# Optimization experiments

Hardware: AMD Instinct MI355X
Metric: run time of the kernel (lower is better)

Reference implementation:

```python
import jax, jax.numpy as jnp
import numpy as np

N = 16384
E = 262144
HID = 128
NFILT = 128
NGAUSS = 50
NINTER = 6
CUTOFF = 10.0
NUMZ = 100
LOG2 = 0.6931471805599453


def ssp(x):
    # ShiftedSoftplus
    return jax.nn.softplus(x) - LOG2


def setup_inputs() -> dict:
    key = jax.random.key(0)
    ks = jax.random.split(key, 20)
    z = jax.random.randint(ks[0], (N,), 0, NUMZ)
    pos = jax.random.uniform(ks[1], (N, 3), dtype=jnp.float32) * 5.0  # box side 5 -> all pairs < cutoff
    edge_index = jax.random.randint(ks[2], (2, E), 0, N)
    s = lambda k, shape, fan: jax.random.normal(k, shape, dtype=jnp.float32) / np.sqrt(fan)
    params = dict(
        emb=s(ks[3], (NUMZ, HID), 1.0),
        Wf1=s(ks[4], (NINTER, NGAUSS, NFILT), NGAUSS), bf1=jnp.zeros((NINTER, NFILT), jnp.float32),
        Wf2=s(ks[5], (NINTER, NFILT, NFILT), NFILT), bf2=jnp.zeros((NINTER, NFILT), jnp.float32),
        Wl1=s(ks[6], (NINTER, HID, NFILT), HID),
        Wl2=s(ks[7], (NINTER, NFILT, HID), NFILT), bl2=jnp.zeros((NINTER, HID), jnp.float32),
        Wl=s(ks[8], (NINTER, HID, HID), HID), bl=jnp.zeros((NINTER, HID), jnp.float32),
        Wo1=s(ks[9], (HID, HID // 2), HID), bo1=jnp.zeros((HID // 2,), jnp.float32),
        Wo2=s(ks[10], (HID // 2, 1), HID // 2), bo2=jnp.zeros((1,), jnp.float32),
    )
    return dict(z=z, pos=pos, edge_index=edge_index, **params)


def reference(z, pos, edge_index, emb, Wf1, bf1, Wf2, bf2, Wl1, Wl2, bl2, Wl, bl, Wo1, bo1, Wo2, bo2):
    src, dst = edge_index[0], edge_index[1]
    # edge distances and Gaussian smearing
    d = jnp.linalg.norm(pos[src] - pos[dst], axis=-1)          # [E]
    offset = jnp.linspace(0.0, CUTOFF, NGAUSS, dtype=jnp.float32)
    coeff = -0.5 / (offset[1] - offset[0]) ** 2
    ea = jnp.exp(coeff * (d[:, None] - offset) ** 2)            # [E, NGAUSS]
    C = 0.5 * (jnp.cos(d * (np.pi / CUTOFF)) + 1.0)             # cosine cutoff [E]

    h = emb[z]                                                  # [N, HID]
    for i in range(NINTER):
        # continuous-filter weights
        Wfilt = (ssp(ea @ Wf1[i] + bf1[i]) @ Wf2[i] + bf2[i]) * C[:, None]  # [E, NFILT]
        x = h @ Wl1[i]                                          # lin1, no bias [N, NFILT]
        msg = x[src] * Wfilt                                    # gather + filter
        agg = jax.ops.segment_sum(msg, dst, num_segments=N)     # scatter-sum [N, NFILT]
        x = ssp(agg @ Wl2[i] + bl2[i]) @ Wl[i] + bl[i]          # lin2 -> ssp -> lin
        h = h + x

    h = ssp(h @ Wo1 + bo1) @ Wo2 + bo2                          # [N, 1] per-atom energy
    out = jnp.sum(h, axis=0, keepdims=True)                     # 'add' readout, single graph -> [1, 1]
    return jax.nn.relu(out)
```

## Files before the change

### kernel.cpp

```cpp
#include <hip/hip_runtime.h>
#include <math.h>

#define NATOM 16384
#define NEDGE 262144
#define HID 128
#define NG 50
#define NI 6

typedef _Float16 h8_t __attribute__((ext_vector_type(8)));
typedef _Float16 h4_t __attribute__((ext_vector_type(4)));
typedef float    f4_t __attribute__((ext_vector_type(4)));

__device__ __forceinline__ float ssp_f(float v) {
    float e = __expf(-fabsf(v));
    return fmaxf(v, 0.0f) + __logf(1.0f + e) - 0.69314718055994531f;
}

__global__ void fill0(float* __restrict__ p, int n4) {
    int i = blockIdx.x * 256 + threadIdx.x;
    if (i < n4) ((float4*)p)[i] = make_float4(0.f, 0.f, 0.f, 0.f);
}

__global__ void hist_k(const int* __restrict__ ei, int* __restrict__ cnt) {
    int e = blockIdx.x * 256 + threadIdx.x;
    if (e < NEDGE) atomicAdd(&cnt[ei[NEDGE + e]], 1);
}

__global__ void scan_k(const int* __restrict__ cnt, int* __restrict__ offs) {
    __shared__ int part[256];
    int t = threadIdx.x;
    int base = t * 64;
    int s = 0;
    for (int i = 0; i < 64; ++i) s += cnt[base + i];
    part[t] = s;
    __syncthreads();
    for (int off = 1; off < 256; off <<= 1) {
        int v = (t >= off) ? part[t - off] : 0;
        __syncthreads();
        part[t] += v;
        __syncthreads();
    }
    int r = part[t] - s;
    for (int i = 0; i < 64; ++i) { offs[base + i] = r; r += cnt[base + i]; }
    if (t == 255) offs[NATOM] = r;
}

__global__ void scatter_k(const int* __restrict__ ei, const int* __restrict__ offs,
                          int* __restrict__ cnt, int* __restrict__ sSrc, int* __restrict__ sDst) {
    int e = blockIdx.x * 256 + threadIdx.x;
    if (e >= NEDGE) return;
    int d = ei[NEDGE + e];
    int r = atomicAdd(&cnt[d], 1);
    int j = offs[d] + r;
    sSrc[j] = ei[e];
    sDst[j] = d;
}

__global__ void edge_pre(const float* __restrict__ pos,
                         const int* __restrict__ sSrc, const int* __restrict__ sDst,
                         _Float16* __restrict__ eaH, _Float16* __restrict__ eaL,
                         float* __restrict__ Cb) {
    int j = blockIdx.x * 256 + threadIdx.x;
    if (j >= NEDGE) return;
    int s = sSrc[j], dd = sDst[j];
    float dx = pos[3*s]   - pos[3*dd];
    float dy = pos[3*s+1] - pos[3*dd+1];
    float dz = pos[3*s+2] - pos[3*dd+2];
    float d = sqrtf(dx*dx + dy*dy + dz*dz);
    Cb[j] = 0.5f * (cosf(d * 0.31415926535897931f) + 1.0f);
    const float delta = 10.0f / 49.0f;
    const float coeff = -0.5f / (delta * delta);
    #pragma unroll
    for (int gq = 0; gq < 8; ++gq) {
        h8_t hv, lv;
        #pragma unroll
        for (int r = 0; r < 8; ++r) {
            int g = gq * 8 + r;
            float v = 0.0f;
            if (g < NG) { float u = d - (float)g * delta; v = __expf(coeff * u * u); }
            _Float16 hh = (_Float16)v;
            hv[r] = hh;
            lv[r] = (_Float16)(v - (float)hh);
        }
        *(h8_t*)&eaH[(size_t)j * 64 + gq * 8] = hv;
        *(h8_t*)&eaL[(size_t)j * 64 + gq * 8] = lv;
    }
}

__global__ void wprep(const float* __restrict__ Wf1, const float* __restrict__ Wf2,
                      const float* __restrict__ Wl1, const float* __restrict__ Wl2,
                      const float* __restrict__ Wl,
                      _Float16* __restrict__ w1h, _Float16* __restrict__ w1l,
                      _Float16* __restrict__ w2h, _Float16* __restrict__ w2l,
                      _Float16* __restrict__ wnh, _Float16* __restrict__ wnl) {
    int idx = blockIdx.x * 256 + threadIdx.x;
    const int S1 = NI * 128 * 64, S2 = NI * 128 * 128;
    if (idx < S1) {
        int i = idx >> 13, r = idx & 8191, fo = r >> 6, k = r & 63;
        float v = (k < NG) ? Wf1[(size_t)i * NG * 128 + k * 128 + fo] : 0.0f;
        _Float16 hh = (_Float16)v;
        w1h[idx] = hh; w1l[idx] = (_Float16)(v - (float)hh);
        return;
    }
    idx -= S1;
    if (idx < S2) {
        int i = idx >> 14, r = idx & 16383, fo = r >> 7, k = r & 127;
        float v = Wf2[(size_t)i * 128 * 128 + k * 128 + fo];
        _Float16 hh = (_Float16)v;
        w2h[idx] = hh; w2l[idx] = (_Float16)(v - (float)hh);
        return;
    }
    idx -= S2;
    if (idx < 3 * S2) {
        int mi = idx >> 14;
        int r = idx & 16383, fo = r >> 7, k = r & 127;
        int m = mi / NI, i = mi % NI;
        const float* W = (m == 0) ? Wl1 : (m == 1) ? Wl2 : Wl;
        float v = W[(size_t)i * 128 * 128 + k * 128 + fo];
        _Float16 hh = (_Float16)v;
        wnh[idx] = hh; wnl[idx] = (_Float16)(v - (float)hh);
    }
}

__global__ void embed_k(const int* __restrict__ z, const float* __restrict__ emb,
                        float* __restrict__ h) {
    int tid = blockIdx.x * 256 + threadIdx.x;
    int n = tid >> 7, f = tid & 127;
    h[tid] = emb[z[n] * HID + f];
}

__launch_bounds__(256)
__global__ void gemm_node_mfma(const float* __restrict__ A,
                               const _Float16* __restrict__ wth, const _Float16* __restrict__ wtl,
                               float* __restrict__ Cout) {
    __shared__ _Float16 aH[64 * 136];
    __shared__ _Float16 aL[64 * 136];
    int t = threadIdx.x;
    int mb = blockIdx.x * 64;
    #pragma unroll
    for (int j = 0; j < 8; ++j) {
        int idx = t + j * 256;
        int row = idx >> 5, c4 = idx & 31;
        f4_t v = *(const f4_t*)&A[(size_t)(mb + row) * HID + c4 * 4];
        h4_t hh, ll;
        #pragma unroll
        for (int r = 0; r < 4; ++r) {
            _Float16 hx = (_Float16)v[r];
            hh[r] = hx; ll[r] = (_Float16)(v[r] - (float)hx);
        }
        *(h4_t*)&aH[row * 136 + c4 * 4] = hh;
        *(h4_t*)&aL[row * 136 + c4 * 4] = ll;
    }
    __syncthreads();

    int wv = t >> 6, lane = t & 63, l15 = lane & 15, quad = lane >> 4;
    f4_t acc[2][4];
    #pragma unroll
    for (int m = 0; m < 2; ++m)
        #pragma unroll
        for (int n = 0; n < 4; ++n) acc[m][n] = (f4_t)0.0f;

    for (int kc = 0; kc < 4; ++kc) {
        int k0 = kc * 32 + quad * 8;
        h8_t a_h[2], a_l[2];
        #pragma unroll
        for (int m = 0; m < 2; ++m) {
            int fr = wv * 32 + m * 16 + l15;
            a_h[m] = *(const h8_t*)&wth[fr * 128 + k0];
            a_l[m] = *(const h8_t*)&wtl[fr * 128 + k0];
        }
        #pragma unroll
        for (int n = 0; n < 4; ++n) {
            int er = n * 16 + l15;
            h8_t b_h = *(const h8_t*)&aH[er * 136 + k0];
            h8_t b_l = *(const h8_t*)&aL[er * 136 + k0];
            #pragma unroll
            for (int m = 0; m < 2; ++m) {
                acc[m][n] = __builtin_amdgcn_mfma_f32_16x16x32_f16(a_h[m], b_h, acc[m][n], 0, 0, 0);
                acc[m][n] = __builtin_amdgcn_mfma_f32_16x16x32_f16(a_h[m], b_l, acc[m][n], 0, 0, 0);
                acc[m][n] = __builtin_amdgcn_mfma_f32_16x16x32_f16(a_l[m], b_h, acc[m][n], 0, 0, 0);
            }
        }
    }

    #pragma unroll
    for (int n = 0; n < 4; ++n) {
        int el = n * 16 + l15;
        size_t row = (size_t)(mb + el);
        #pragma unroll
        for (int m = 0; m < 2; ++m) {
            int fb = wv * 32 + m * 16 + quad * 4;
            f4_t o;
            #pragma unroll
            for (int r = 0; r < 4; ++r) o[r] = acc[m][n][r];
            *(f4_t*)&Cout[row * 128 + fb] = o;
        }
    }
}

__launch_bounds__(256)
__global__ void gemm_node2(const float* __restrict__ agg,
                           const _Float16* __restrict__ w2th, const _Float16* __restrict__ w2tl,
                           const _Float16* __restrict__ wlth, const _Float16* __restrict__ wltl,
                           const float* __restrict__ bl2, const float* __restrict__ bl,
                           float* __restrict__ h) {
    __shared__ _Float16 aH[64 * 136];
    __shared__ _Float16 aL[64 * 136];
    int t = threadIdx.x;
    int mb = blockIdx.x * 64;
    #pragma unroll
    for (int j = 0; j < 8; ++j) {
        int idx = t + j * 256;
        int row = idx >> 5, c4 = idx & 31;
        f4_t v = *(const f4_t*)&agg[(size_t)(mb + row) * HID + c4 * 4];
        h4_t hh, ll;
        #pragma unroll
        for (int r = 0; r < 4; ++r) {
            _Float16 hx = (_Float16)v[r];
            hh[r] = hx; ll[r] = (_Float16)(v[r] - (float)hx);
        }
        *(h4_t*)&aH[row * 136 + c4 * 4] = hh;
        *(h4_t*)&aL[row * 136 + c4 * 4] = ll;
    }
    __syncthreads();

    int wv = t >> 6, lane = t & 63, l15 = lane & 15, quad = lane >> 4;
    int fq = wv * 32 + quad * 4;
    f4_t acc[2][4];

    #pragma unroll
    for (int m = 0; m < 2; ++m)
        #pragma unroll
        for (int n = 0; n < 4; ++n) acc[m][n] = (f4_t)0.0f;
    for (int kc = 0; kc < 4; ++kc) {
        int k0 = kc * 32 + quad * 8;
        h8_t a_h[2], a_l[2];
        #pragma unroll
        for (int m = 0; m < 2; ++m) {
            int fr = wv * 32 + m * 16 + l15;
            a_h[m] = *(const h8_t*)&w2th[fr * 128 + k0];
            a_l[m] = *(const h8_t*)&w2tl[fr * 128 + k0];
        }
        #pragma unroll
        for (int n = 0; n < 4; ++n) {
            int er = n * 16 + l15;
            h8_t b_h = *(const h8_t*)&aH[er * 136 + k0];
            h8_t b_l = *(const h8_t*)&aL[er * 136 + k0];
            #pragma unroll
            for (int m = 0; m < 2; ++m) {
                acc[m][n] = __builtin_amdgcn_mfma_f32_16x16x32_f16(a_h[m], b_h, acc[m][n], 0, 0, 0);
                acc[m][n] = __builtin_amdgcn_mfma_f32_16x16x32_f16(a_h[m], b_l, acc[m][n], 0, 0, 0);
                acc[m][n] = __builtin_amdgcn_mfma_f32_16x16x32_f16(a_l[m], b_h, acc[m][n], 0, 0, 0);
            }
        }
    }
    f4_t b2v[2];
    b2v[0] = *(const f4_t*)&bl2[fq]; b2v[1] = *(const f4_t*)&bl2[fq + 16];
    __syncthreads();

    #pragma unroll
    for (int m = 0; m < 2; ++m)
        #pragma unroll
        for (int n = 0; n < 4; ++n) {
            int el = n * 16 + l15;
            int fb = wv * 32 + m * 16 + quad * 4;
            h4_t hh, ll;
            #pragma unroll
            for (int r = 0; r < 4; ++r) {
                float sv = ssp_f(acc[m][n][r] + b2v[m][r]);
                _Float16 hx = (_Float16)sv;
                hh[r] = hx;
                ll[r] = (_Float16)(sv - (float)hx);
            }
            *(h4_t*)&aH[el * 136 + fb] = hh;
            *(h4_t*)&aL[el * 136 + fb] = ll;
        }
    __syncthreads();

    #pragma unroll
    for (int m = 0; m < 2; ++m)
        #pragma unroll
        for (int n = 0; n < 4; ++n) acc[m][n] = (f4_t)0.0f;
    for (int kc = 0; kc < 4; ++kc) {
        int k0 = kc * 32 + quad * 8;
        h8_t a_h[2], a_l[2];
        #pragma unroll
        for (int m = 0; m < 2; ++m) {
            int fr = wv * 32 + m * 16 + l15;
            a_h[m] = *(const h8_t*)&wlth[fr * 128 + k0];
            a_l[m] = *(const h8_t*)&wltl[fr * 128 + k0];
        }
        #pragma unroll
        for (int n = 0; n < 4; ++n) {
            int er = n * 16 + l15;
            h8_t b_h = *(const h8_t*)&aH[er * 136 + k0];
            h8_t b_l = *(const h8_t*)&aL[er * 136 + k0];
            #pragma unroll
            for (int m = 0; m < 2; ++m) {
                acc[m][n] = __builtin_amdgcn_mfma_f32_16x16x32_f16(a_h[m], b_h, acc[m][n], 0, 0, 0);
                acc[m][n] = __builtin_amdgcn_mfma_f32_16x16x32_f16(a_h[m], b_l, acc[m][n], 0, 0, 0);
                acc[m][n] = __builtin_amdgcn_mfma_f32_16x16x32_f16(a_l[m], b_h, acc[m][n], 0, 0, 0);
            }
        }
    }
    f4_t blv[2];
    blv[0] = *(const f4_t*)&bl[fq]; blv[1] = *(const f4_t*)&bl[fq + 16];

    #pragma unroll
    for (int n = 0; n < 4; ++n) {
        int el = n * 16 + l15;
        size_t row = (size_t)(mb + el);
        #pragma unroll
        for (int m = 0; m < 2; ++m) {
            int fb = wv * 32 + m * 16 + quad * 4;
            f4_t hv = *(const f4_t*)&h[row * 128 + fb];
            f4_t o;
            #pragma unroll
            for (int r = 0; r < 4; ++r) o[r] = hv[r] + acc[m][n][r] + blv[m][r];
            *(f4_t*)&h[row * 128 + fb] = o;
        }
    }
}

#define T1_LDW 136
#define MROW 132

__launch_bounds__(256)
__global__ void edge_filter(const float* __restrict__ x, float* __restrict__ agg,
                            const int* __restrict__ sSrc, const int* __restrict__ sDst,
                            const float* __restrict__ Cb,
                            const _Float16* __restrict__ eaH, const _Float16* __restrict__ eaL,
                            const _Float16* __restrict__ w1h, const _Float16* __restrict__ w1l,
                            const _Float16* __restrict__ w2h, const _Float16* __restrict__ w2l,
                            const float* __restrict__ bf1, const float* __restrict__ bf2) {
    __shared__ __align__(16) unsigned char smem[34816];
    __shared__ float cL[64];
    __shared__ int dstl[64];
    __shared__ int srcl[64];

    _Float16* t1H = (_Float16*)smem;
    _Float16* t1L = (_Float16*)(smem + 17408);
    float*    msg = (float*)smem;

    int t = threadIdx.x;
    int eb = blockIdx.x * 64;
    int wv = t >> 6, lane = t & 63;
    int l15 = lane & 15, quad = lane >> 4;

    if (t < 64) {
        int e = eb + t;
        srcl[t] = sSrc[e];
        dstl[t] = sDst[e];
        cL[t] = Cb[e];
    }

    int fq = wv*32 + quad*4;
    f4_t b1v[2], b2v[2];
    b1v[0] = *(const f4_t*)&bf1[fq];  b1v[1] = *(const f4_t*)&bf1[fq + 16];
    b2v[0] = *(const f4_t*)&bf2[fq];  b2v[1] = *(const f4_t*)&bf2[fq + 16];

    f4_t acc1[2][4];
    #pragma unroll
    for (int m = 0; m < 2; ++m)
        #pragma unroll
        for (int n = 0; n < 4; ++n) acc1[m][n] = (f4_t)0.0f;

    #pragma unroll
    for (int kc = 0; kc < 2; ++kc) {
        int k0 = kc*32 + quad*8;
        h8_t a_h[2], a_l[2], b_h[4], b_l[4];
        #pragma unroll
        for (int m = 0; m < 2; ++m) {
            int fr = wv*32 + m*16 + l15;
            a_h[m] = *(const h8_t*)&w1h[fr*64 + k0];
            a_l[m] = *(const h8_t*)&w1l[fr*64 + k0];
        }
        #pragma unroll
        for (int n = 0; n < 4; ++n) {
            size_t er = (size_t)(eb + n*16 + l15);
            b_h[n] = *(const h8_t*)&eaH[er*64 + k0];
            b_l[n] = *(const h8_t*)&eaL[er*64 + k0];
        }
        #pragma unroll
        for (int m = 0; m < 2; ++m)
            #pragma unroll
            for (int n = 0; n < 4; ++n) {
                acc1[m][n] = __builtin_amdgcn_mfma_f32_16x16x32_f16(a_h[m], b_h[n], acc1[m][n], 0, 0, 0);
                acc1[m][n] = __builtin_amdgcn_mfma_f32_16x16x32_f16(a_h[m], b_l[n], acc1[m][n], 0, 0, 0);
                acc1[m][n] = __builtin_amdgcn_mfma_f32_16x16x32_f16(a_l[m], b_h[n], acc1[m][n], 0, 0, 0);
            }
    }

    #pragma unroll
    for (int m = 0; m < 2; ++m)
        #pragma unroll
        for (int n = 0; n < 4; ++n) {
            int el = n*16 + l15;
            int fb = wv*32 + m*16 + quad*4;
            h4_t hh, ll;
            #pragma unroll
            for (int r = 0; r < 4; ++r) {
                float sv = ssp_f(acc1[m][n][r] + b1v[m][r]);
                _Float16 hx = (_Float16)sv;
                hh[r] = hx;
                ll[r] = (_Float16)(sv - (float)hx);
            }
            *(h4_t*)&t1H[el*T1_LDW + fb] = hh;
            *(h4_t*)&t1L[el*T1_LDW + fb] = ll;
        }
    __syncthreads();

    f4_t acc2[2][4];
    #pragma unroll
    for (int m = 0; m < 2; ++m)
        #pragma unroll
        for (int n = 0; n < 4; ++n) acc2[m][n] = (f4_t)0.0f;

    for (int kc = 0; kc < 4; ++kc) {
        int k0 = kc*32 + quad*8;
        h8_t a_h[2], a_l[2];
        #pragma unroll
        for (int m = 0; m < 2; ++m) {
            int fr = wv*32 + m*16 + l15;
            a_h[m] = *(const h8_t*)&w2h[fr*128 + k0];
            a_l[m] = *(const h8_t*)&w2l[fr*128 + k0];
        }
        #pragma unroll
        for (int n = 0; n < 4; ++n) {
            int er = n*16 + l15;
            h8_t b_h = *(const h8_t*)&t1H[er*T1_LDW + k0];
            h8_t b_l = *(const h8_t*)&t1L[er*T1_LDW + k0];
            #pragma unroll
            for (int m = 0; m < 2; ++m) {
                acc2[m][n] = __builtin_amdgcn_mfma_f32_16x16x32_f16(a_h[m], b_h, acc2[m][n], 0, 0, 0);
                acc2[m][n] = __builtin_amdgcn_mfma_f32_16x16x32_f16(a_h[m], b_l, acc2[m][n], 0, 0, 0);
                acc2[m][n] = __builtin_amdgcn_mfma_f32_16x16x32_f16(a_l[m], b_h, acc2[m][n], 0, 0, 0);
            }
        }
    }
    __syncthreads();

    #pragma unroll
    for (int n = 0; n < 4; ++n) {
        int el = n*16 + l15;
        float ce = cL[el];
        int s = srcl[el];
        #pragma unroll
        for (int m = 0; m < 2; ++m) {
            int fb = wv*32 + m*16 + quad*4;
            f4_t xr = *(const f4_t*)&x[(size_t)s * HID + fb];
            f4_t o;
            #pragma unroll
            for (int r = 0; r < 4; ++r)
                o[r] = (acc2[m][n][r] + b2v[m][r]) * ce * xr[r];
            *(f4_t*)&msg[el*MROW + fb] = o;
        }
    }
    __syncthreads();

    int f = t & 127, hf = t >> 7;
    int ib = hf * 32;
    float run = 0.0f;
    int cur = dstl[ib];
    for (int i = ib; i < ib + 32; ++i) {
        int dnow = dstl[i];
        if (dnow != cur) {
            atomicAdd(&agg[(size_t)cur * HID + f], run);
            run = 0.0f;
            cur = dnow;
        }
        run += msg[i*MROW + f];
    }
    atomicAdd(&agg[(size_t)cur * HID + f], run);
}

__launch_bounds__(256)
__global__ void readout1(const float* __restrict__ h, const float* __restrict__ Wo1,
                         const float* __restrict__ bo1, const float* __restrict__ Wo2,
                         const float* __restrict__ bo2, float* __restrict__ accum) {
    __shared__ float w1[128 * 64];
    __shared__ float part[4];
    int t = threadIdx.x;
    for (int i = t; i < 128 * 16; i += 256)
        ((float4*)w1)[i] = ((const float4*)Wo1)[i];
    __syncthreads();
    int f = t & 63, wv = t >> 6;
    float b = bo1[f], w2v = Wo2[f];
    float lsum = 0.0f;
    for (int a = 0; a < 16; ++a) {
        int n = blockIdx.x * 64 + wv * 16 + a;
        const float* hr = &h[(size_t)n * HID];
        float acc = b;
        #pragma unroll 16
        for (int k = 0; k < 128; ++k)
            acc = fmaf(hr[k], w1[k*64 + f], acc);
        lsum += ssp_f(acc) * w2v;
    }
    #pragma unroll
    for (int off = 32; off > 0; off >>= 1)
        lsum += __shfl_down(lsum, off, 64);
    if (f == 0) part[wv] = lsum;
    __syncthreads();
    if (t == 0)
        atomicAdd(accum, part[0] + part[1] + part[2] + part[3] + 64.0f * bo2[0]);
}

__global__ void readout2(const float* __restrict__ accum, float* __restrict__ out) {
    out[0] = fmaxf(accum[0], 0.0f);
}

extern "C" void kernel_launch(void* const* d_in, const int* in_sizes, int n_in,
                              void* d_out, int out_size, void* d_ws, size_t ws_size,
                              hipStream_t stream) {
    const int*   z   = (const int*)d_in[0];
    const float* pos = (const float*)d_in[1];
    const int*   ei  = (const int*)d_in[2];
    const float* emb = (const float*)d_in[3];
    const float* Wf1 = (const float*)d_in[4];
    const float* bf1 = (const float*)d_in[5];
    const float* Wf2 = (const float*)d_in[6];
    const float* bf2 = (const float*)d_in[7];
    const float* Wl1 = (const float*)d_in[8];
    const float* Wl2 = (const float*)d_in[9];
    const float* bl2 = (const float*)d_in[10];
    const float* Wl  = (const float*)d_in[11];
    const float* bl  = (const float*)d_in[12];
    const float* Wo1 = (const float*)d_in[13];
    const float* bo1 = (const float*)d_in[14];
    const float* Wo2 = (const float*)d_in[15];
    const float* bo2 = (const float*)d_in[16];
    float* out = (float*)d_out;

    _Float16* w1h = (_Float16*)d_ws;
    _Float16* w1l = w1h + NI * 8192;
    _Float16* w2h = w1l + NI * 8192;
    _Float16* w2l = w2h + NI * 16384;
    _Float16* wnh = w2l + NI * 16384;
    _Float16* wnl = wnh + 3 * NI * 16384;
    _Float16* eaH = wnl + 3 * NI * 16384;
    _Float16* eaL = eaH + (size_t)NEDGE * 64;
    float* Cb  = (float*)(eaL + (size_t)NEDGE * 64);
    float* h   = Cb + NEDGE;
    float* x   = h   + (size_t)NATOM * HID;
    float* agg = x   + (size_t)NATOM * HID;
    float* accum = agg + (size_t)NATOM * HID;
    int* cnt  = (int*)(accum + 4);
    int* offs = cnt + NATOM;
    int* sSrc = offs + NATOM + 4;
    int* sDst = sSrc + NEDGE;

    fill0<<<NATOM/4/256, 256, 0, stream>>>((float*)cnt, NATOM/4);
    hist_k<<<NEDGE/256, 256, 0, stream>>>(ei, cnt);
    scan_k<<<1, 256, 0, stream>>>(cnt, offs);
    fill0<<<NATOM/4/256, 256, 0, stream>>>((float*)cnt, NATOM/4);
    scatter_k<<<NEDGE/256, 256, 0, stream>>>(ei, offs, cnt, sSrc, sDst);

    edge_pre<<<NEDGE/256, 256, 0, stream>>>(pos, sSrc, sDst, eaH, eaL, Cb);
    wprep<<<(NI*8192 + NI*16384 + 3*NI*16384)/256, 256, 0, stream>>>(
        Wf1, Wf2, Wl1, Wl2, Wl, w1h, w1l, w2h, w2l, wnh, wnl);
    embed_k<<<(NATOM*HID)/256, 256, 0, stream>>>(z, emb, h);

    for (int i = 0; i < NI; ++i) {
        gemm_node_mfma<<<256, 256, 0, stream>>>(h, wnh + (size_t)(0*NI+i)*16384,
            wnl + (size_t)(0*NI+i)*16384, x);
        fill0<<<(NATOM*HID/4)/256, 256, 0, stream>>>(agg, NATOM*HID/4);
        edge_filter<<<NEDGE/64, 256, 0, stream>>>(x, agg, sSrc, sDst, Cb, eaH, eaL,
            w1h + (size_t)i*8192, w1l + (size_t)i*8192,
            w2h + (size_t)i*16384, w2l + (size_t)i*16384,
            bf1 + i*HID, bf2 + i*HID);
        gemm_node2<<<256, 256, 0, stream>>>(agg,
            wnh + (size_t)(1*NI+i)*16384, wnl + (size_t)(1*NI+i)*16384,
            wnh + (size_t)(2*NI+i)*16384, wnl + (size_t)(2*NI+i)*16384,
            bl2 + i*HID, bl + i*HID, h);
    }
    fill0<<<1, 256, 0, stream>>>(accum, 1);
    readout1<<<NATOM/64, 256, 0, stream>>>(h, Wo1, bo1, Wo2, bo2, accum);
    readout2<<<1, 1, 0, stream>>>(accum, out);
}
```

Baseline: 916.7 us.

## Fuse next lin1 into node GEMM and make edge filter persistent with prefetch

The node-update kernel now also computes the next interaction's lin1 (h @ Wl1) from the freshly updated h kept in shared memory. This removes a separate gemm_node_mfma launch per iteration and a re-read of h. The edge_filter kernel now processes 4 edge tiles per block and keeps the filter weights in registers across tiles. It stages edge features through shared memory with register prefetch of the next tile and issues the x gathers early to overlap with MFMA work. In exchange, register pressure rises (launch bounds of 2 blocks), shared memory use grows, and there are fewer blocks to spread across the device.

```diff
diff --git a/kernel.cpp b/kernel.cpp
--- a/kernel.cpp
+++ b/kernel.cpp
@@ -199,11 +199,12 @@
 }
 
 __launch_bounds__(256)
-__global__ void gemm_node2(const float* __restrict__ agg,
+__global__ void gemm_node3(const float* __restrict__ agg,
                            const _Float16* __restrict__ w2th, const _Float16* __restrict__ w2tl,
                            const _Float16* __restrict__ wlth, const _Float16* __restrict__ wltl,
+                           const _Float16* __restrict__ w1nh, const _Float16* __restrict__ w1nl,
                            const float* __restrict__ bl2, const float* __restrict__ bl,
-                           float* __restrict__ h) {
+                           float* __restrict__ h, float* __restrict__ x) {
     __shared__ _Float16 aH[64 * 136];
     __shared__ _Float16 aL[64 * 136];
     int t = threadIdx.x;
@@ -305,6 +306,7 @@
     }
     f4_t blv[2];
     blv[0] = *(const f4_t*)&bl[fq]; blv[1] = *(const f4_t*)&bl[fq + 16];
+    __syncthreads();
 
     #pragma unroll
     for (int n = 0; n < 4; ++n) {
@@ -315,17 +317,67 @@
             int fb = wv * 32 + m * 16 + quad * 4;
             f4_t hv = *(const f4_t*)&h[row * 128 + fb];
             f4_t o;
-            #pragma unroll
-            for (int r = 0; r < 4; ++r) o[r] = hv[r] + acc[m][n][r] + blv[m][r];
+            h4_t hh, ll;
+            #pragma unroll
+            for (int r = 0; r < 4; ++r) {
+                o[r] = hv[r] + acc[m][n][r] + blv[m][r];
+                _Float16 hx = (_Float16)o[r];
+                hh[r] = hx; ll[r] = (_Float16)(o[r] - (float)hx);
+            }
             *(f4_t*)&h[row * 128 + fb] = o;
+            *(h4_t*)&aH[el * 136 + fb] = hh;
+            *(h4_t*)&aL[el * 136 + fb] = ll;
+        }
+    }
+    if (!w1nh) return;
+    __syncthreads();
+
+    #pragma unroll
+    for (int m = 0; m < 2; ++m)
+        #pragma unroll
+        for (int n = 0; n < 4; ++n) acc[m][n] = (f4_t)0.0f;
+    for (int kc = 0; kc < 4; ++kc) {
+        int k0 = kc * 32 + quad * 8;
+        h8_t a_h[2], a_l[2];
+        #pragma unroll
+        for (int m = 0; m < 2; ++m) {
+            int fr = wv * 32 + m * 16 + l15;
+            a_h[m] = *(const h8_t*)&w1nh[fr * 128 + k0];
+            a_l[m] = *(const h8_t*)&w1nl[fr * 128 + k0];
+        }
+        #pragma unroll
+        for (int n = 0; n < 4; ++n) {
+            int er = n * 16 + l15;
+            h8_t b_h = *(const h8_t*)&aH[er * 136 + k0];
+            h8_t b_l = *(const h8_t*)&aL[er * 136 + k0];
+            #pragma unroll
+            for (int m = 0; m < 2; ++m) {
+                acc[m][n] = __builtin_amdgcn_mfma_f32_16x16x32_f16(a_h[m], b_h, acc[m][n], 0, 0, 0);
+                acc[m][n] = __builtin_amdgcn_mfma_f32_16x16x32_f16(a_h[m], b_l, acc[m][n], 0, 0, 0);
+                acc[m][n] = __builtin_amdgcn_mfma_f32_16x16x32_f16(a_l[m], b_h, acc[m][n], 0, 0, 0);
+            }
+        }
+    }
+    #pragma unroll
+    for (int n = 0; n < 4; ++n) {
+        int el = n * 16 + l15;
+        size_t row = (size_t)(mb + el);
+        #pragma unroll
+        for (int m = 0; m < 2; ++m) {
+            int fb = wv * 32 + m * 16 + quad * 4;
+            f4_t o;
+            #pragma unroll
+            for (int r = 0; r < 4; ++r) o[r] = acc[m][n][r];
+            *(f4_t*)&x[row * 128 + fb] = o;
         }
     }
 }
 
 #define T1_LDW 136
 #define MROW 132
-
-__launch_bounds__(256)
+#define EF_TPB 4
+
+__launch_bounds__(256, 2)
 __global__ void edge_filter(const float* __restrict__ x, float* __restrict__ agg,
                             const int* __restrict__ sSrc, const int* __restrict__ sDst,
                             const float* __restrict__ Cb,
@@ -333,145 +385,205 @@
                             const _Float16* __restrict__ w1h, const _Float16* __restrict__ w1l,
                             const _Float16* __restrict__ w2h, const _Float16* __restrict__ w2l,
                             const float* __restrict__ bf1, const float* __restrict__ bf2) {
-    __shared__ __align__(16) unsigned char smem[34816];
+    __shared__ __align__(16) _Float16 eaHs[64 * 72];
+    __shared__ __align__(16) _Float16 eaLs[64 * 72];
+    __shared__ __align__(16) unsigned char t1mem[34816];
     __shared__ float cL[64];
     __shared__ int dstl[64];
     __shared__ int srcl[64];
 
-    _Float16* t1H = (_Float16*)smem;
-    _Float16* t1L = (_Float16*)(smem + 17408);
-    float*    msg = (float*)smem;
+    _Float16* t1H = (_Float16*)t1mem;
+    _Float16* t1L = (_Float16*)(t1mem + 17408);
+    float*    msg = (float*)t1mem;
 
     int t = threadIdx.x;
-    int eb = blockIdx.x * 64;
     int wv = t >> 6, lane = t & 63;
     int l15 = lane & 15, quad = lane >> 4;
-
-    if (t < 64) {
-        int e = eb + t;
-        srcl[t] = sSrc[e];
-        dstl[t] = sDst[e];
-        cL[t] = Cb[e];
-    }
-
-    int fq = wv*32 + quad*4;
+    int tile0 = blockIdx.x * EF_TPB;
+
+    h8_t w1fh[2][2], w1fl[2][2], w2fh[4][2], w2fl[4][2];
+    #pragma unroll
+    for (int kc = 0; kc < 2; ++kc) {
+        int k0 = kc * 32 + quad * 8;
+        #pragma unroll
+        for (int m = 0; m < 2; ++m) {
+            int fr = wv * 32 + m * 16 + l15;
+            w1fh[kc][m] = *(const h8_t*)&w1h[fr * 64 + k0];
+            w1fl[kc][m] = *(const h8_t*)&w1l[fr * 64 + k0];
+        }
+    }
+    #pragma unroll
+    for (int kc = 0; kc < 4; ++kc) {
+        int k0 = kc * 32 + quad * 8;
+        #pragma unroll
+        for (int m = 0; m < 2; ++m) {
+            int fr = wv * 32 + m * 16 + l15;
+            w2fh[kc][m] = *(const h8_t*)&w2h[fr * 128 + k0];
+            w2fl[kc][m] = *(const h8_t*)&w2l[fr * 128 + k0];
+        }
+    }
+    int fq = wv * 32 + quad * 4;
     f4_t b1v[2], b2v[2];
     b1v[0] = *(const f4_t*)&bf1[fq];  b1v[1] = *(const f4_t*)&bf1[fq + 16];
     b2v[0] = *(const f4_t*)&bf2[fq];  b2v[1] = *(const f4_t*)&bf2[fq + 16];
 
-    f4_t acc1[2][4];
-    #pragma unroll
-    for (int m = 0; m < 2; ++m)
-        #pragma unroll
-        for (int n = 0; n < 4; ++n) acc1[m][n] = (f4_t)0.0f;
-
-    #pragma unroll
-    for (int kc = 0; kc < 2; ++kc) {
-        int k0 = kc*32 + quad*8;
-        h8_t a_h[2], a_l[2], b_h[4], b_l[4];
-        #pragma unroll
-        for (int m = 0; m < 2; ++m) {
-            int fr = wv*32 + m*16 + l15;
-            a_h[m] = *(const h8_t*)&w1h[fr*64 + k0];
-            a_l[m] = *(const h8_t*)&w1l[fr*64 + k0];
-        }
+    {
+        int eb = tile0 * 64;
+        if (t < 64) {
+            srcl[t] = sSrc[eb + t];
+            dstl[t] = sDst[eb + t];
+            cL[t]   = Cb[eb + t];
+        }
+        #pragma unroll
+        for (int c = 0; c < 4; ++c) {
+            int ch = t + c * 256;
+            int pl = ch >> 9, rem = ch & 511, e = rem >> 3, ks = rem & 7;
+            h8_t v = *(const h8_t*)((pl ? eaL : eaH) + (size_t)(eb + e) * 64 + ks * 8);
+            *(h8_t*)((pl ? eaLs : eaHs) + e * 72 + ks * 8) = v;
+        }
+    }
+    __syncthreads();
+
+    for (int tt = 0; tt < EF_TPB; ++tt) {
+        if (tt > 0) {
+            __syncthreads();
+            if (t < 64) {
+                int e = (tile0 + tt) * 64 + t;
+                srcl[t] = sSrc[e];
+                dstl[t] = sDst[e];
+                cL[t]   = Cb[e];
+            }
+        }
+        bool pre = (tt < EF_TPB - 1);
+        h8_t sreg[4];
+        if (pre) {
+            int ebn = (tile0 + tt + 1) * 64;
+            #pragma unroll
+            for (int c = 0; c < 4; ++c) {
+                int ch = t + c * 256;
+                int pl = ch >> 9, rem = ch & 511, e = rem >> 3, ks = rem & 7;
+                sreg[c] = *(const h8_t*)((pl ? eaL : eaH) + (size_t)(ebn + e) * 64 + ks * 8);
+            }
+        }
+
+        f4_t acc1[2][4];
+        #pragma unroll
+        for (int m = 0; m < 2; ++m)
+            #pragma unroll
+            for (int n = 0; n < 4; ++n) acc1[m][n] = (f4_t)0.0f;
+        #pragma unroll
+        for (int kc = 0; kc < 2; ++kc) {
+            int k0 = kc * 32 + quad * 8;
+            h8_t b_h[4], b_l[4];
+            #pragma unroll
+            for (int n = 0; n < 4; ++n) {
+                int er = n * 16 + l15;
+                b_h[n] = *(const h8_t*)&eaHs[er * 72 + k0];
+                b_l[n] = *(const h8_t*)&eaLs[er * 72 + k0];
+            }
+            #pragma unroll
+            for (int m = 0; m < 2; ++m)
+                #pragma unroll
+                for (int n = 0; n < 4; ++n) {
+                    acc1[m][n] = __builtin_amdgcn_mfma_f32_16x16x32_f16(w1fh[kc][m], b_h[n], acc1[m][n], 0, 0, 0);
+                    acc1[m][n] = __builtin_amdgcn_mfma_f32_16x16x32_f16(w1fh[kc][m], b_l[n], acc1[m][n], 0, 0, 0);
+                    acc1[m][n] = __builtin_amdgcn_mfma_f32_16x16x32_f16(w1fl[kc][m], b_h[n], acc1[m][n], 0, 0, 0);
+                }
+        }
+
+        #pragma unroll
+        for (int m = 0; m < 2; ++m)
+            #pragma unroll
+            for (int n = 0; n < 4; ++n) {
+                int el = n * 16 + l15;
+                int fb = wv * 32 + m * 16 + quad * 4;
+                h4_t hh, ll;
+                #pragma unroll
+                for (int r = 0; r < 4; ++r) {
+                    float sv = ssp_f(acc1[m][n][r] + b1v[m][r]);
+                    _Float16 hx = (_Float16)sv;
+                    hh[r] = hx;
+                    ll[r] = (_Float16)(sv - (float)hx);
+                }
+                *(h4_t*)&t1H[el * T1_LDW + fb] = hh;
+                *(h4_t*)&t1L[el * T1_LDW + fb] = ll;
+            }
+        __syncthreads();
+
+        if (pre) {
+            #pragma unroll
+            for (int c = 0; c < 4; ++c) {
+                int ch = t + c * 256;
+                int pl = ch >> 9, rem = ch & 511, e = rem >> 3, ks = rem & 7;
+                *(h8_t*)((pl ? eaLs : eaHs) + e * 72 + ks * 8) = sreg[c];
+            }
+        }
+        f4_t xr[4][2];
         #pragma unroll
         for (int n = 0; n < 4; ++n) {
-            size_t er = (size_t)(eb + n*16 + l15);
-            b_h[n] = *(const h8_t*)&eaH[er*64 + k0];
-            b_l[n] = *(const h8_t*)&eaL[er*64 + k0];
-        }
+            int el = n * 16 + l15;
+            int s = srcl[el];
+            #pragma unroll
+            for (int m = 0; m < 2; ++m) {
+                int fb = wv * 32 + m * 16 + quad * 4;
+                xr[n][m] = *(const f4_t*)&x[(size_t)s * HID + fb];
+            }
+        }
+
+        f4_t acc2[2][4];
         #pragma unroll
         for (int m = 0; m < 2; ++m)
             #pragma unroll
+            for (int n = 0; n < 4; ++n) acc2[m][n] = (f4_t)0.0f;
+        #pragma unroll
+        for (int kc = 0; kc < 4; ++kc) {
+            int k0 = kc * 32 + quad * 8;
+            #pragma unroll
             for (int n = 0; n < 4; ++n) {
-                acc1[m][n] = __builtin_amdgcn_mfma_f32_16x16x32_f16(a_h[m], b_h[n], acc1[m][n], 0, 0, 0);
-                acc1[m][n] = __builtin_amdgcn_mfma_f32_16x16x32_f16(a_h[m], b_l[n], acc1[m][n], 0, 0, 0);
-                acc1[m][n] = __builtin_amdgcn_mfma_f32_16x16x32_f16(a_l[m], b_h[n], acc1[m][n], 0, 0, 0);
-            }
-    }
-
-    #pragma unroll
-    for (int m = 0; m < 2; ++m)
+                int er = n * 16 + l15;
+                h8_t b_h = *(const h8_t*)&t1H[er * T1_LDW + k0];
+                h8_t b_l = *(const h8_t*)&t1L[er * T1_LDW + k0];
+                #pragma unroll
+                for (int m = 0; m < 2; ++m) {
+                    acc2[m][n] = __builtin_amdgcn_mfma_f32_16x16x32_f16(w2fh[kc][m], b_h, acc2[m][n], 0, 0, 0);
+                    acc2[m][n] = __builtin_amdgcn_mfma_f32_16x16x32_f16(w2fh[kc][m], b_l, acc2[m][n], 0, 0, 0);
+                    acc2[m][n] = __builtin_amdgcn_mfma_f32_16x16x32_f16(w2fl[kc][m], b_h, acc2[m][n], 0, 0, 0);
+                }
+            }
+        }
+        __syncthreads();
+
         #pragma unroll
         for (int n = 0; n < 4; ++n) {
-            int el = n*16 + l15;
-            int fb = wv*32 + m*16 + quad*4;
-            h4_t hh, ll;
-            #pragma unroll
-            for (int r = 0; r < 4; ++r) {
-                float sv = ssp_f(acc1[m][n][r] + b1v[m][r]);
-                _Float16 hx = (_Float16)sv;
-                hh[r] = hx;
-                ll[r] = (_Float16)(sv - (float)hx);
-            }
-            *(h4_t*)&t1H[el*T1_LDW + fb] = hh;
-            *(h4_t*)&t1L[el*T1_LDW + fb] = ll;
-        }
-    __syncthreads();
-
-    f4_t acc2[2][4];
-    #pragma unroll
-    for (int m = 0; m < 2; ++m)
-        #pragma unroll
-        for (int n = 0; n < 4; ++n) acc2[m][n] = (f4_t)0.0f;
-
-    for (int kc = 0; kc < 4; ++kc) {
-        int k0 = kc*32 + quad*8;
-        h8_t a_h[2], a_l[2];
-        #pragma unroll
-        for (int m = 0; m < 2; ++m) {
-            int fr = wv*32 + m*16 + l15;
-            a_h[m] = *(const h8_t*)&w2h[fr*128 + k0];
-            a_l[m] = *(const h8_t*)&w2l[fr*128 + k0];
-        }
-        #pragma unroll
-        for (int n = 0; n < 4; ++n) {
-            int er = n*16 + l15;
-            h8_t b_h = *(const h8_t*)&t1H[er*T1_LDW + k0];
-            h8_t b_l = *(const h8_t*)&t1L[er*T1_LDW + k0];
+            int el = n * 16 + l15;
+            float ce = cL[el];
             #pragma unroll
             for (int m = 0; m < 2; ++m) {
-                acc2[m][n] = __builtin_amdgcn_mfma_f32_16x16x32_f16(a_h[m], b_h, acc2[m][n], 0, 0, 0);
-                acc2[m][n] = __builtin_amdgcn_mfma_f32_16x16x32_f16(a_h[m], b_l, acc2[m][n], 0, 0, 0);
-                acc2[m][n] = __builtin_amdgcn_mfma_f32_16x16x32_f16(a_l[m], b_h, acc2[m][n], 0, 0, 0);
-            }
-        }
-    }
-    __syncthreads();
-
-    #pragma unroll
-    for (int n = 0; n < 4; ++n) {
-        int el = n*16 + l15;
-        float ce = cL[el];
-        int s = srcl[el];
-        #pragma unroll
-        for (int m = 0; m < 2; ++m) {
-            int fb = wv*32 + m*16 + quad*4;
-            f4_t xr = *(const f4_t*)&x[(size_t)s * HID + fb];
-            f4_t o;
-            #pragma unroll
-            for (int r = 0; r < 4; ++r)
-                o[r] = (acc2[m][n][r] + b2v[m][r]) * ce * xr[r];
-            *(f4_t*)&msg[el*MROW + fb] = o;
-        }
-    }
-    __syncthreads();
-
-    int f = t & 127, hf = t >> 7;
-    int ib = hf * 32;
-    float run = 0.0f;
-    int cur = dstl[ib];
-    for (int i = ib; i < ib + 32; ++i) {
-        int dnow = dstl[i];
-        if (dnow != cur) {
-            atomicAdd(&agg[(size_t)cur * HID + f], run);
-            run = 0.0f;
-            cur = dnow;
-        }
-        run += msg[i*MROW + f];
-    }
-    atomicAdd(&agg[(size_t)cur * HID + f], run);
+                int fb = wv * 32 + m * 16 + quad * 4;
+                f4_t o;
+                #pragma unroll
+                for (int r = 0; r < 4; ++r)
+                    o[r] = (acc2[m][n][r] + b2v[m][r]) * ce * xr[n][m][r];
+                *(f4_t*)&msg[el * MROW + fb] = o;
+            }
+        }
+        __syncthreads();
+
+        int f = t & 127, hf = t >> 7;
+        int ib = hf * 32;
+        float run = 0.0f;
+        int cur = dstl[ib];
+        for (int i = ib; i < ib + 32; ++i) {
+            int dnow = dstl[i];
+            if (dnow != cur) {
+                atomicAdd(&agg[(size_t)cur * HID + f], run);
+                run = 0.0f;
+                cur = dnow;
+            }
+            run += msg[i * MROW + f];
+        }
+        atomicAdd(&agg[(size_t)cur * HID + f], run);
+    }
 }
 
 __launch_bounds__(256)
@@ -560,18 +672,20 @@
         Wf1, Wf2, Wl1, Wl2, Wl, w1h, w1l, w2h, w2l, wnh, wnl);
     embed_k<<<(NATOM*HID)/256, 256, 0, stream>>>(z, emb, h);
 
+    gemm_node_mfma<<<256, 256, 0, stream>>>(h, wnh + (size_t)0*16384,
+        wnl + (size_t)0*16384, x);
     for (int i = 0; i < NI; ++i) {
-        gemm_node_mfma<<<256, 256, 0, stream>>>(h, wnh + (size_t)(0*NI+i)*16384,
-            wnl + (size_t)(0*NI+i)*16384, x);
         fill0<<<(NATOM*HID/4)/256, 256, 0, stream>>>(agg, NATOM*HID/4);
-        edge_filter<<<NEDGE/64, 256, 0, stream>>>(x, agg, sSrc, sDst, Cb, eaH, eaL,
+        edge_filter<<<NEDGE/64/EF_TPB, 256, 0, stream>>>(x, agg, sSrc, sDst, Cb, eaH, eaL,
             w1h + (size_t)i*8192, w1l + (size_t)i*8192,
             w2h + (size_t)i*16384, w2l + (size_t)i*16384,
             bf1 + i*HID, bf2 + i*HID);
-        gemm_node2<<<256, 256, 0, stream>>>(agg,
+        const _Float16* w1nh = (i < NI-1) ? wnh + (size_t)(i+1)*16384 : nullptr;
+        const _Float16* w1nl = (i < NI-1) ? wnl + (size_t)(i+1)*16384 : nullptr;
+        gemm_node3<<<256, 256, 0, stream>>>(agg,
             wnh + (size_t)(1*NI+i)*16384, wnl + (size_t)(1*NI+i)*16384,
             wnh + (size_t)(2*NI+i)*16384, wnl + (size_t)(2*NI+i)*16384,
-            bl2 + i*HID, bl + i*HID, h);
+            w1nh, w1nl, bl2 + i*HID, bl + i*HID, h, x);
     }
     fill0<<<1, 256, 0, stream>>>(accum, 1);
     readout1<<<NATOM/64, 256, 0, stream>>>(h, Wo1, bo1, Wo2, bo2, accum);
```

Result: faster. 791.3 us (-13.7%).
